# Kernel optimization log

Measured on AMD Instinct MI355X. Metric: run time of the kernel, lower is better.

Reference implementation:

```python
import jax, jax.numpy as jnp
import numpy as np

L, B, H, P = 2048, 16, 512, 256
EPS = 1e-6  # flax nnx LayerNorm default


def setup_inputs() -> dict:
    key = jax.random.key(0)
    ks = jax.random.split(key, 12)
    x = jax.random.normal(ks[0], (L, B, H), jnp.float32)
    d = jax.random.bernoulli(ks[1], 0.01, (L, B))  # sparse reset signal
    hidden_re = jnp.zeros((1, B, P), jnp.float32)
    hidden_im = jnp.zeros((1, B, P), jnp.float32)
    # S5 diagonal state matrix (stable: Re < 0)
    Lambda_re = -0.5 * jnp.exp(0.5 * jax.random.normal(ks[2], (P,), jnp.float32))
    Lambda_im = np.float32(np.pi) * jax.random.normal(ks[3], (P,), jnp.float32)
    B_re = jax.random.normal(ks[4], (P, H), jnp.float32) / np.sqrt(2.0 * H).astype(np.float32)
    B_im = jax.random.normal(ks[5], (P, H), jnp.float32) / np.sqrt(2.0 * H).astype(np.float32)
    C_re = jax.random.normal(ks[6], (H, P), jnp.float32) / np.sqrt(P).astype(np.float32)
    C_im = jax.random.normal(ks[7], (H, P), jnp.float32) / np.sqrt(P).astype(np.float32)
    D = jax.random.normal(ks[8], (H,), jnp.float32)
    log_step = jax.random.uniform(ks[9], (P,), jnp.float32,
                                  minval=np.log(1e-3).astype(np.float32),
                                  maxval=np.log(1e-1).astype(np.float32))
    ln_scale = jnp.ones((H,), jnp.float32)
    ln_bias = jnp.zeros((H,), jnp.float32)
    out2_w = jax.random.normal(ks[10], (H, H), jnp.float32) / np.sqrt(H).astype(np.float32)
    out2_b = jnp.zeros((H,), jnp.float32)
    return dict(x=x, d=d, hidden_re=hidden_re, hidden_im=hidden_im,
                Lambda_re=Lambda_re, Lambda_im=Lambda_im, B_re=B_re, B_im=B_im,
                C_re=C_re, C_im=C_im, D=D, log_step=log_step,
                ln_scale=ln_scale, ln_bias=ln_bias, out2_w=out2_w, out2_b=out2_b)


def reference(x, d, hidden_re, hidden_im, Lambda_re, Lambda_im, B_re, B_im,
              C_re, C_im, D, log_step, ln_scale, ln_bias, out2_w, out2_b):
    def ln(v):
        mu = v.mean(-1, keepdims=True)
        var = v.var(-1, keepdims=True)
        return (v - mu) * jax.lax.rsqrt(var + EPS) * ln_scale + ln_bias

    skip = x
    xn = ln(x)  # prenorm

    # --- S5 SSM (ZOH discretization), vmapped over batch == vectorized over axis 1 ---
    step = jnp.exp(log_step)  # step_rescale = 1.0
    Lam = (Lambda_re + 1j * Lambda_im).astype(jnp.complex64)          # (P,)
    Lam_bar = jnp.exp(Lam * step.astype(jnp.complex64))                # (P,)
    B_bar = ((Lam_bar - 1.0) / Lam)[:, None] * (B_re + 1j * B_im).astype(jnp.complex64)  # (P,H)
    Bu = jnp.einsum('lbh,ph->lbp', xn.astype(jnp.complex64), B_bar)    # (L,B,P)

    keep = (1.0 - d.astype(jnp.float32)).astype(jnp.complex64)         # reset zeroes the carry
    a = Lam_bar[None, None, :] * keep[:, :, None]                      # (L,B,P)
    h0 = (hidden_re + 1j * hidden_im).astype(jnp.complex64)[0]         # (B,P)
    Bu = Bu.at[0].add(a[0] * h0)                                       # fold in initial hidden

    def binop(e1, e2):
        a1, b1 = e1
        a2, b2 = e2
        return (a2 * a1, a2 * b1 + b2)

    _, xs = jax.lax.associative_scan(binop, (a, Bu), axis=0)           # (L,B,P) states
    Cmat = (C_re + 1j * C_im).astype(jnp.complex64)
    ys = 2.0 * jnp.einsum('lbp,hp->lbh', xs, Cmat).real + D * xn       # conj-sym readout + feedthrough
    new_hidden = xs[-1:]                                               # (1,B,P)

    y = ln(ys)  # gtrxl norm (shared LayerNorm)
    # half_glu2: x * sigmoid(W2 gelu(x) + b2)
    x1 = jax.nn.gelu(y)  # approximate=True matches nnx.gelu
    y = y * jax.nn.sigmoid(x1 @ out2_w + out2_b)
    out = skip + y
    return (new_hidden.real, new_hidden.imag, out)
```

## Files before the change

kernel.cpp:

```cpp
#include <hip/hip_runtime.h>

#define LL 2048
#define BB 16
#define HH 512
#define PP 256
#define MM (LL*BB)
#define NN 512
#define KK 512
#define NC 64
#define CLEN 32

typedef __bf16 bf16x8 __attribute__((ext_vector_type(8)));
typedef float  f32x4  __attribute__((ext_vector_type(4)));

__device__ __forceinline__ unsigned short f2bf(float f) {
  unsigned u = __builtin_bit_cast(unsigned, f);
  u = (u + 0x7fffu + ((u >> 16) & 1u)) >> 16;
  return (unsigned short)u;
}
__device__ __forceinline__ float bf2f(unsigned short s) {
  unsigned u = ((unsigned)s) << 16;
  return __builtin_bit_cast(float, u);
}

__global__ void detect_kernel(const unsigned int* __restrict__ dw, int* __restrict__ flag) {
  __shared__ int sInt, sFloat;
  if (threadIdx.x == 0) { sInt = 1; sFloat = 1; }
  __syncthreads();
  int allInt = 1, allFloat = 1;
  for (int i = threadIdx.x; i < 8192; i += 256) {
    unsigned v = dw[i];
    if (v > 1u) allInt = 0;
    if (v != 0u && v != 0x3f800000u) allFloat = 0;
  }
  if (!allInt) atomicAnd(&sInt, 0);
  if (!allFloat) atomicAnd(&sFloat, 0);
  __syncthreads();
  if (threadIdx.x == 0) *flag = sInt ? 0 : (sFloat ? 1 : 2);
}

__device__ __forceinline__ float keep_val(const void* d, int flag, int idx) {
  if (flag == 0) return 1.f - (float)((const int*)d)[idx];
  if (flag == 1) return 1.f - ((const float*)d)[idx];
  return 1.f - (float)((const unsigned char*)d)[idx];
}

__global__ void precompute_kernel(
    const float* __restrict__ Lre, const float* __restrict__ Lim,
    const float* __restrict__ Bre, const float* __restrict__ Bim,
    const float* __restrict__ Cre, const float* __restrict__ Cim,
    const float* __restrict__ lstep, const float* __restrict__ w2,
    unsigned short* __restrict__ W1t, unsigned short* __restrict__ W2t,
    unsigned short* __restrict__ W3t, float* __restrict__ lam_re,
    float* __restrict__ lam_im) {
  int t = blockIdx.x * 256 + threadIdx.x;
  int k = t & (KK - 1);
  int n = t >> 9;
  {
    int p = n & (PP - 1);
    float lr = Lre[p], li = Lim[p];
    float st = expf(lstep[p]);
    float er = expf(lr * st);
    float ang = li * st;
    float lbr = er * cosf(ang), lbi = er * sinf(ang);
    float den = lr * lr + li * li;
    float wr = ((lbr - 1.f) * lr + lbi * li) / den;
    float wi = (lbi * lr - (lbr - 1.f) * li) / den;
    float br = Bre[p * HH + k], bi = Bim[p * HH + k];
    float v = (n < PP) ? (wr * br - wi * bi) : (wr * bi + wi * br);
    W1t[(size_t)n * KK + k] = f2bf(v);
  }
  {
    float v = (k < PP) ? (2.f * Cre[n * PP + k]) : (-2.f * Cim[n * PP + (k - PP)]);
    W2t[(size_t)n * KK + k] = f2bf(v);
  }
  W3t[(size_t)n * KK + k] = f2bf(w2[(size_t)k * HH + n]);
  if (t < PP) {
    float lr = Lre[t], li = Lim[t];
    float st = expf(lstep[t]);
    float er = expf(lr * st);
    float ang = li * st;
    lam_re[t] = er * cosf(ang);
    lam_im[t] = er * sinf(ang);
  }
}

__global__ void ln1_kernel(const float* __restrict__ x, const float* __restrict__ sc,
                           const float* __restrict__ bs, unsigned short* __restrict__ xn) {
  int row = blockIdx.x * 4 + (threadIdx.x >> 6);
  int lane = threadIdx.x & 63;
  const float4* xr = (const float4*)(x + (size_t)row * HH) + lane * 2;
  float4 a = xr[0], b = xr[1];
  float s = (a.x + a.y) + (a.z + a.w) + (b.x + b.y) + (b.z + b.w);
  float q = a.x * a.x + a.y * a.y + a.z * a.z + a.w * a.w +
            b.x * b.x + b.y * b.y + b.z * b.z + b.w * b.w;
#pragma unroll
  for (int off = 32; off; off >>= 1) { s += __shfl_xor(s, off); q += __shfl_xor(q, off); }
  float mean = s * (1.f / HH);
  float var = fmaxf(q * (1.f / HH) - mean * mean, 0.f);
  float rstd = rsqrtf(var + 1e-6f);
  const float4* scp = (const float4*)sc + lane * 2;
  const float4* bsp = (const float4*)bs + lane * 2;
  float4 s0 = scp[0], s1 = scp[1], b0 = bsp[0], b1 = bsp[1];
  unsigned short o[8];
  o[0] = f2bf((a.x - mean) * rstd * s0.x + b0.x);
  o[1] = f2bf((a.y - mean) * rstd * s0.y + b0.y);
  o[2] = f2bf((a.z - mean) * rstd * s0.z + b0.z);
  o[3] = f2bf((a.w - mean) * rstd * s0.w + b0.w);
  o[4] = f2bf((b.x - mean) * rstd * s1.x + b1.x);
  o[5] = f2bf((b.y - mean) * rstd * s1.y + b1.y);
  o[6] = f2bf((b.z - mean) * rstd * s1.z + b1.z);
  o[7] = f2bf((b.w - mean) * rstd * s1.w + b1.w);
  uint4 pk;
  pk.x = o[0] | ((unsigned)o[1] << 16);
  pk.y = o[2] | ((unsigned)o[3] << 16);
  pk.z = o[4] | ((unsigned)o[5] << 16);
  pk.w = o[6] | ((unsigned)o[7] << 16);
  *((uint4*)(xn + (size_t)row * HH) + lane) = pk;
}

__global__ void ln2_kernel(const float* __restrict__ ys, const float* __restrict__ sc,
                           const float* __restrict__ bs, unsigned short* __restrict__ y,
                           unsigned short* __restrict__ x1) {
  int row = blockIdx.x * 4 + (threadIdx.x >> 6);
  int lane = threadIdx.x & 63;
  const float4* xr = (const float4*)(ys + (size_t)row * HH) + lane * 2;
  float4 a = xr[0], b = xr[1];
  float s = (a.x + a.y) + (a.z + a.w) + (b.x + b.y) + (b.z + b.w);
  float q = a.x * a.x + a.y * a.y + a.z * a.z + a.w * a.w +
            b.x * b.x + b.y * b.y + b.z * b.z + b.w * b.w;
#pragma unroll
  for (int off = 32; off; off >>= 1) { s += __shfl_xor(s, off); q += __shfl_xor(q, off); }
  float mean = s * (1.f / HH);
  float var = fmaxf(q * (1.f / HH) - mean * mean, 0.f);
  float rstd = rsqrtf(var + 1e-6f);
  const float4* scp = (const float4*)sc + lane * 2;
  const float4* bsp = (const float4*)bs + lane * 2;
  float4 s0 = scp[0], s1 = scp[1], b0 = bsp[0], b1 = bsp[1];
  float v[8] = { a.x, a.y, a.z, a.w, b.x, b.y, b.z, b.w };
  float scv[8] = { s0.x, s0.y, s0.z, s0.w, s1.x, s1.y, s1.z, s1.w };
  float bsv[8] = { b0.x, b0.y, b0.z, b0.w, b1.x, b1.y, b1.z, b1.w };
  unsigned short oy[8], og[8];
#pragma unroll
  for (int j = 0; j < 8; j++) {
    float yv = (v[j] - mean) * rstd * scv[j] + bsv[j];
    oy[j] = f2bf(yv);
    float g = 0.5f * yv * (1.f + tanhf(0.7978845608f * (yv + 0.044715f * yv * yv * yv)));
    og[j] = f2bf(g);
  }
  uint4 py, pg;
  py.x = oy[0] | ((unsigned)oy[1] << 16); py.y = oy[2] | ((unsigned)oy[3] << 16);
  py.z = oy[4] | ((unsigned)oy[5] << 16); py.w = oy[6] | ((unsigned)oy[7] << 16);
  pg.x = og[0] | ((unsigned)og[1] << 16); pg.y = og[2] | ((unsigned)og[3] << 16);
  pg.z = og[4] | ((unsigned)og[5] << 16); pg.w = og[6] | ((unsigned)og[7] << 16);
  *((uint4*)(y  + (size_t)row * HH) + lane) = py;
  *((uint4*)(x1 + (size_t)row * HH) + lane) = pg;
}

template <int EPI>
__global__ __launch_bounds__(256, 2) void gemm_kernel(
    const unsigned short* __restrict__ A, const unsigned short* __restrict__ Wt,
    float* __restrict__ Cout, const float* __restrict__ Dvec,
    const unsigned short* __restrict__ aux16, const float* __restrict__ skip) {
  __shared__ alignas(16) unsigned short lA[128 * 64];
  __shared__ alignas(16) unsigned short lB[128 * 64];
  int tid = threadIdx.x;
  int w = tid >> 6, lane = tid & 63;
  int m0 = blockIdx.y * 128, n0 = blockIdx.x * 128;
  int wr = w >> 1, wc = w & 1;
  f32x4 acc[4][4];
#pragma unroll
  for (int i = 0; i < 4; i++)
#pragma unroll
    for (int j = 0; j < 4; j++) acc[i][j] = (f32x4){0.f, 0.f, 0.f, 0.f};

  for (int kt = 0; kt < KK / 64; ++kt) {
    __syncthreads();
#pragma unroll
    for (int i = 0; i < 4; i++) {
      int idx = i * 256 + tid;
      int r = idx >> 3, c = idx & 7;
      const unsigned short* g = A + (size_t)(m0 + r) * KK + kt * 64 + c * 8;
      unsigned short* l = &lA[(i * 256 + w * 64) * 8];
      __builtin_amdgcn_global_load_lds((const __attribute__((address_space(1))) void*)g,
                                       (__attribute__((address_space(3))) void*)l, 16, 0, 0);
    }
#pragma unroll
    for (int i = 0; i < 4; i++) {
      int idx = i * 256 + tid;
      int r = idx >> 3, c = idx & 7;
      const unsigned short* g = Wt + (size_t)(n0 + r) * KK + kt * 64 + c * 8;
      unsigned short* l = &lB[(i * 256 + w * 64) * 8];
      __builtin_amdgcn_global_load_lds((const __attribute__((address_space(1))) void*)g,
                                       (__attribute__((address_space(3))) void*)l, 16, 0, 0);
    }
    __syncthreads();
#pragma unroll
    for (int ks = 0; ks < 2; ++ks) {
      bf16x8 aF[4], bF[4];
#pragma unroll
      for (int m = 0; m < 4; m++)
        aF[m] = *reinterpret_cast<const bf16x8*>(
            &lA[(wr * 64 + m * 16 + (lane & 15)) * 64 + ks * 32 + (lane >> 4) * 8]);
#pragma unroll
      for (int n = 0; n < 4; n++)
        bF[n] = *reinterpret_cast<const bf16x8*>(
            &lB[(wc * 64 + n * 16 + (lane & 15)) * 64 + ks * 32 + (lane >> 4) * 8]);
#pragma unroll
      for (int m = 0; m < 4; m++)
#pragma unroll
        for (int n = 0; n < 4; n++)
          acc[m][n] = __builtin_amdgcn_mfma_f32_16x16x32_bf16(aF[m], bF[n], acc[m][n], 0, 0, 0);
    }
  }
  int lr4 = (lane >> 4) * 4, lc = lane & 15;
#pragma unroll
  for (int m = 0; m < 4; m++) {
    int rowb = m0 + wr * 64 + m * 16 + lr4;
#pragma unroll
    for (int n = 0; n < 4; n++) {
      int col = n0 + wc * 64 + n * 16 + lc;
#pragma unroll
      for (int j = 0; j < 4; j++) {
        int row = rowb + j;
        size_t idx = (size_t)row * NN + col;
        float v = acc[m][n][j];
        if (EPI == 0) {
          Cout[idx] = v;
        } else if (EPI == 1) {
          Cout[idx] = v + Dvec[col] * bf2f(aux16[idx]);
        } else {
          float z = v + Dvec[col];
          float sg = 1.f / (1.f + expf(-z));
          Cout[idx] = skip[idx] + bf2f(aux16[idx]) * sg;
        }
      }
    }
  }
}

__global__ void scanA_kernel(const float* __restrict__ Bu, const void* __restrict__ d,
                             const int* __restrict__ dflag, const float* __restrict__ lam_re,
                             const float* __restrict__ lam_im, float* __restrict__ Ar,
                             float* __restrict__ Ai, float* __restrict__ Sr,
                             float* __restrict__ Si) {
  int bx = blockIdx.x;
  int c = bx >> 4, b = bx & 15;
  int p = threadIdx.x;
  int fl = *dflag;
  float lr = lam_re[p], li = lam_im[p];
  float Apr = 1.f, Api = 0.f, sr = 0.f, si = 0.f;
  int l0 = c * CLEN;
  for (int j = 0; j < CLEN; j++) {
    int l = l0 + j;
    float kp = keep_val(d, fl, l * BB + b);
    float ar = lr * kp, ai = li * kp;
    size_t ro = (size_t)(l * BB + b) * NN;
    float bur = Bu[ro + p], bui = Bu[ro + PP + p];
    float nsr = ar * sr - ai * si + bur;
    float nsi = ar * si + ai * sr + bui;
    sr = nsr; si = nsi;
    float nar = ar * Apr - ai * Api;
    float nai = ar * Api + ai * Apr;
    Apr = nar; Api = nai;
  }
  int o = bx * PP + p;
  Ar[o] = Apr; Ai[o] = Api; Sr[o] = sr; Si[o] = si;
}

__global__ void scanB_kernel(const float* __restrict__ hr0, const float* __restrict__ hi0,
                             const float* __restrict__ Ar, const float* __restrict__ Ai,
                             const float* __restrict__ Sr, const float* __restrict__ Si,
                             float* __restrict__ Cr, float* __restrict__ Ci,
                             float* __restrict__ outHid) {
  int b = blockIdx.x;
  int p = threadIdx.x;
  float cr = hr0[b * PP + p], ci = hi0[b * PP + p];
  for (int c = 0; c < NC; c++) {
    int o = (c * BB + b) * PP + p;
    Cr[o] = cr; Ci[o] = ci;
    float ar = Ar[o], ai = Ai[o];
    float nr = ar * cr - ai * ci + Sr[o];
    float ni = ar * ci + ai * cr + Si[o];
    cr = nr; ci = ni;
  }
  outHid[b * PP + p] = cr;
  outHid[BB * PP + b * PP + p] = ci;
}

__global__ void scanC_kernel(const float* __restrict__ Bu, const void* __restrict__ d,
                             const int* __restrict__ dflag, const float* __restrict__ lam_re,
                             const float* __restrict__ lam_im, const float* __restrict__ Cr,
                             const float* __restrict__ Ci, unsigned short* __restrict__ xs) {
  int bx = blockIdx.x;
  int c = bx >> 4, b = bx & 15;
  int p = threadIdx.x;
  int fl = *dflag;
  float lr = lam_re[p], li = lam_im[p];
  float hr = Cr[bx * PP + p], hi = Ci[bx * PP + p];
  int l0 = c * CLEN;
  for (int j = 0; j < CLEN; j++) {
    int l = l0 + j;
    float kp = keep_val(d, fl, l * BB + b);
    float ar = lr * kp, ai = li * kp;
    size_t ro = (size_t)(l * BB + b) * NN;
    float bur = Bu[ro + p], bui = Bu[ro + PP + p];
    float nhr = ar * hr - ai * hi + bur;
    float nhi = ar * hi + ai * hr + bui;
    hr = nhr; hi = nhi;
    xs[ro + p] = f2bf(hr);
    xs[ro + PP + p] = f2bf(hi);
  }
}

extern "C" void kernel_launch(void* const* d_in, const int* in_sizes, int n_in,
                              void* d_out, int out_size, void* d_ws, size_t ws_size,
                              hipStream_t stream) {
  const float* x    = (const float*)d_in[0];
  const void*  dmask= d_in[1];
  const float* hidr = (const float*)d_in[2];
  const float* hidi = (const float*)d_in[3];
  const float* Lre  = (const float*)d_in[4];
  const float* Lim  = (const float*)d_in[5];
  const float* Bre  = (const float*)d_in[6];
  const float* Bim  = (const float*)d_in[7];
  const float* Cre  = (const float*)d_in[8];
  const float* Cim  = (const float*)d_in[9];
  const float* Dv   = (const float*)d_in[10];
  const float* lst  = (const float*)d_in[11];
  const float* lsc  = (const float*)d_in[12];
  const float* lbs  = (const float*)d_in[13];
  const float* w2   = (const float*)d_in[14];
  const float* b2   = (const float*)d_in[15];
  float* out = (float*)d_out;

  char* ws = (char*)d_ws;
  size_t off = 0;
  auto alloc = [&](size_t bytes) -> void* {
    void* p = ws + off;
    off += (bytes + 255) & ~(size_t)255;
    return p;
  };
  unsigned short* xn  = (unsigned short*)alloc((size_t)MM * KK * 2);
  unsigned short* xs  = (unsigned short*)alloc((size_t)MM * KK * 2);
  float* Bu           = (float*)alloc((size_t)MM * NN * 4);
  unsigned short* W1t = (unsigned short*)alloc((size_t)NN * KK * 2);
  unsigned short* W2t = (unsigned short*)alloc((size_t)NN * KK * 2);
  unsigned short* W3t = (unsigned short*)alloc((size_t)NN * KK * 2);
  float* lam_re = (float*)alloc(PP * 4);
  float* lam_im = (float*)alloc(PP * 4);
  float* Ar = (float*)alloc((size_t)NC * BB * PP * 4);
  float* Ai = (float*)alloc((size_t)NC * BB * PP * 4);
  float* Sr = (float*)alloc((size_t)NC * BB * PP * 4);
  float* Si = (float*)alloc((size_t)NC * BB * PP * 4);
  float* Cr = (float*)alloc((size_t)NC * BB * PP * 4);
  float* Ci = (float*)alloc((size_t)NC * BB * PP * 4);
  int* dflag = (int*)alloc(256);
  unsigned short* y  = xn;
  unsigned short* x1 = xs;
  float* ysb = Bu;

  detect_kernel<<<1, 256, 0, stream>>>((const unsigned int*)dmask, dflag);
  precompute_kernel<<<1024, 256, 0, stream>>>(Lre, Lim, Bre, Bim, Cre, Cim, lst, w2,
                                              W1t, W2t, W3t, lam_re, lam_im);
  ln1_kernel<<<MM / 4, 256, 0, stream>>>(x, lsc, lbs, xn);
  gemm_kernel<0><<<dim3(4, 256), 256, 0, stream>>>(xn, W1t, Bu, nullptr, nullptr, nullptr);
  scanA_kernel<<<NC * BB, 256, 0, stream>>>(Bu, dmask, dflag, lam_re, lam_im, Ar, Ai, Sr, Si);
  scanB_kernel<<<BB, 256, 0, stream>>>(hidr, hidi, Ar, Ai, Sr, Si, Cr, Ci, out);
  scanC_kernel<<<NC * BB, 256, 0, stream>>>(Bu, dmask, dflag, lam_re, lam_im, Cr, Ci, xs);
  gemm_kernel<1><<<dim3(4, 256), 256, 0, stream>>>(xs, W2t, ysb, Dv, xn, nullptr);
  ln2_kernel<<<MM / 4, 256, 0, stream>>>(ysb, lsc, lbs, y, x1);
  gemm_kernel<2><<<dim3(4, 256), 256, 0, stream>>>(x1, W3t, out + 2 * BB * PP, b2, y, x);
}
```

Baseline: 232.7 us.

## Swizzle GEMM LDS tiles, remap workgroups per XCD, raise occupancy bound

The GEMM's LDS tiles get an XOR swizzle on 16-byte chunks, applied both when loading from global into LDS and when reading fragments, to cut bank conflicts on the MFMA operand reads. The grid becomes 1D, and workgroup IDs are remapped so that each XCD (round-robin dispatch over 8) handles a contiguous band of M rows. The intent is better L2 locality for shared A rows. The launch bound rises from 2 to 4 workgroups per CU, which may force register limits and cause spills.

```diff
diff --git a/kernel.cpp b/kernel.cpp
--- a/kernel.cpp
+++ b/kernel.cpp
@@ -158,7 +158,7 @@
 }
 
 template <int EPI>
-__global__ __launch_bounds__(256, 2) void gemm_kernel(
+__global__ __launch_bounds__(256, 4) void gemm_kernel(
     const unsigned short* __restrict__ A, const unsigned short* __restrict__ Wt,
     float* __restrict__ Cout, const float* __restrict__ Dvec,
     const unsigned short* __restrict__ aux16, const float* __restrict__ skip) {
@@ -166,7 +166,10 @@
   __shared__ alignas(16) unsigned short lB[128 * 64];
   int tid = threadIdx.x;
   int w = tid >> 6, lane = tid & 63;
-  int m0 = blockIdx.y * 128, n0 = blockIdx.x * 128;
+  int wgid = blockIdx.x;
+  int xcd = wgid & 7, idx = wgid >> 3;
+  int m0 = (xcd * 32 + (idx >> 2)) * 128;
+  int n0 = (idx & 3) * 128;
   int wr = w >> 1, wc = w & 1;
   f32x4 acc[4][4];
 #pragma unroll
@@ -178,18 +181,20 @@
     __syncthreads();
 #pragma unroll
     for (int i = 0; i < 4; i++) {
-      int idx = i * 256 + tid;
-      int r = idx >> 3, c = idx & 7;
-      const unsigned short* g = A + (size_t)(m0 + r) * KK + kt * 64 + c * 8;
+      int sidx = i * 256 + tid;
+      int r = sidx >> 3, c = sidx & 7;
+      int cs = c ^ (r & 7);
+      const unsigned short* g = A + (size_t)(m0 + r) * KK + kt * 64 + cs * 8;
       unsigned short* l = &lA[(i * 256 + w * 64) * 8];
       __builtin_amdgcn_global_load_lds((const __attribute__((address_space(1))) void*)g,
                                        (__attribute__((address_space(3))) void*)l, 16, 0, 0);
     }
 #pragma unroll
     for (int i = 0; i < 4; i++) {
-      int idx = i * 256 + tid;
-      int r = idx >> 3, c = idx & 7;
-      const unsigned short* g = Wt + (size_t)(n0 + r) * KK + kt * 64 + c * 8;
+      int sidx = i * 256 + tid;
+      int r = sidx >> 3, c = sidx & 7;
+      int cs = c ^ (r & 7);
+      const unsigned short* g = Wt + (size_t)(n0 + r) * KK + kt * 64 + cs * 8;
       unsigned short* l = &lB[(i * 256 + w * 64) * 8];
       __builtin_amdgcn_global_load_lds((const __attribute__((address_space(1))) void*)g,
                                        (__attribute__((address_space(3))) void*)l, 16, 0, 0);
@@ -199,13 +204,17 @@
     for (int ks = 0; ks < 2; ++ks) {
       bf16x8 aF[4], bF[4];
 #pragma unroll
-      for (int m = 0; m < 4; m++)
-        aF[m] = *reinterpret_cast<const bf16x8*>(
-            &lA[(wr * 64 + m * 16 + (lane & 15)) * 64 + ks * 32 + (lane >> 4) * 8]);
-#pragma unroll
-      for (int n = 0; n < 4; n++)
-        bF[n] = *reinterpret_cast<const bf16x8*>(
-            &lB[(wc * 64 + n * 16 + (lane & 15)) * 64 + ks * 32 + (lane >> 4) * 8]);
+      for (int m = 0; m < 4; m++) {
+        int row = wr * 64 + m * 16 + (lane & 15);
+        int s = ks * 4 + (lane >> 4);
+        aF[m] = *reinterpret_cast<const bf16x8*>(&lA[row * 64 + (s ^ (row & 7)) * 8]);
+      }
+#pragma unroll
+      for (int n = 0; n < 4; n++) {
+        int row = wc * 64 + n * 16 + (lane & 15);
+        int s = ks * 4 + (lane >> 4);
+        bF[n] = *reinterpret_cast<const bf16x8*>(&lB[row * 64 + (s ^ (row & 7)) * 8]);
+      }
 #pragma unroll
       for (int m = 0; m < 4; m++)
 #pragma unroll
@@ -223,16 +232,16 @@
 #pragma unroll
       for (int j = 0; j < 4; j++) {
         int row = rowb + j;
-        size_t idx = (size_t)row * NN + col;
+        size_t idxo = (size_t)row * NN + col;
         float v = acc[m][n][j];
         if (EPI == 0) {
-          Cout[idx] = v;
+          Cout[idxo] = v;
         } else if (EPI == 1) {
-          Cout[idx] = v + Dvec[col] * bf2f(aux16[idx]);
+          Cout[idxo] = v + Dvec[col] * bf2f(aux16[idxo]);
         } else {
           float z = v + Dvec[col];
           float sg = 1.f / (1.f + expf(-z));
-          Cout[idx] = skip[idx] + bf2f(aux16[idx]) * sg;
+          Cout[idxo] = skip[idxo] + bf2f(aux16[idxo]) * sg;
         }
       }
     }
@@ -364,11 +373,11 @@
   precompute_kernel<<<1024, 256, 0, stream>>>(Lre, Lim, Bre, Bim, Cre, Cim, lst, w2,
                                               W1t, W2t, W3t, lam_re, lam_im);
   ln1_kernel<<<MM / 4, 256, 0, stream>>>(x, lsc, lbs, xn);
-  gemm_kernel<0><<<dim3(4, 256), 256, 0, stream>>>(xn, W1t, Bu, nullptr, nullptr, nullptr);
+  gemm_kernel<0><<<1024, 256, 0, stream>>>(xn, W1t, Bu, nullptr, nullptr, nullptr);
   scanA_kernel<<<NC * BB, 256, 0, stream>>>(Bu, dmask, dflag, lam_re, lam_im, Ar, Ai, Sr, Si);
   scanB_kernel<<<BB, 256, 0, stream>>>(hidr, hidi, Ar, Ai, Sr, Si, Cr, Ci, out);
   scanC_kernel<<<NC * BB, 256, 0, stream>>>(Bu, dmask, dflag, lam_re, lam_im, Cr, Ci, xs);
-  gemm_kernel<1><<<dim3(4, 256), 256, 0, stream>>>(xs, W2t, ysb, Dv, xn, nullptr);
+  gemm_kernel<1><<<1024, 256, 0, stream>>>(xs, W2t, ysb, Dv, xn, nullptr);
   ln2_kernel<<<MM / 4, 256, 0, stream>>>(ysb, lsc, lbs, y, x1);
-  gemm_kernel<2><<<dim3(4, 256), 256, 0, stream>>>(x1, W3t, out + 2 * BB * PP, b2, y, x);
-}
+  gemm_kernel<2><<<1024, 256, 0, stream>>>(x1, W3t, out + 2 * BB * PP, b2, y, x);
+}
```

After: 221.6 us. 4.7% less time.
